# Kernel tuning notes

Hardware: AMD Instinct MI355X
Metric: run time of the kernel (lower is better)

## Reference

```python
import jax, jax.numpy as jnp
import numpy as np

B, T, C, H = 4, 4096, 2048, 128  # batch, seq, emb_dim, head_size


def setup_inputs() -> dict:
    key = jax.random.key(0)
    k1, k2, k3, k4 = jax.random.split(key, 4)
    idx = jax.random.normal(k1, (B, T, C), dtype=jnp.float32)
    # nn.Linear weight layout: [out_features, in_features]; scale like torch init
    s = 1.0 / np.sqrt(C)
    Wq = jax.random.uniform(k2, (H, C), jnp.float32, -s, s)
    Wk = jax.random.uniform(k3, (H, C), jnp.float32, -s, s)
    Wv = jax.random.uniform(k4, (H, C), jnp.float32, -s, s)
    return {"idx": idx, "Wq": Wq, "Wk": Wk, "Wv": Wv}


def reference(idx, Wq, Wk, Wv):
    b, t, c = idx.shape
    q = jnp.einsum('btc,hc->bth', idx, Wq)  # [B,T,H]
    k = jnp.einsum('btc,hc->bth', idx, Wk)
    v = jnp.einsum('btc,hc->bth', idx, Wv)
    # NOTE: original computes keys @ queries^T and scales by emb_dim**-0.5
    scale = jnp.asarray(c, idx.dtype) ** -0.5
    wei = jnp.einsum('bih,bjh->bij', k, q) * scale  # [B,T,T]
    causal = jnp.tril(jnp.ones((t, t), dtype=bool))
    wei = jnp.where(causal, wei, -jnp.inf)
    wei = jax.nn.softmax(wei, axis=-1)
    return jnp.einsum('bij,bjh->bih', wei, v)  # [B,T,H]
```

## Files before the change

kernel.cpp:

```cpp
#include <hip/hip_runtime.h>
#include <hip/hip_bf16.h>
#include <cstdint>

#define TSEQ 4096
#define CDIM 2048
#define HDIM 128

typedef short bf8v __attribute__((ext_vector_type(8)));
typedef float f4v  __attribute__((ext_vector_type(4)));

__device__ __forceinline__ unsigned short f2b(float f) {
  union { float f; unsigned u; } v; v.f = f;
  unsigned u = v.u;
  return (unsigned short)((u + 0x7fffu + ((u >> 16) & 1u)) >> 16);
}

__device__ __forceinline__ f4v mfma16(bf8v a, bf8v b, f4v c) {
  return __builtin_amdgcn_mfma_f32_16x16x32_bf16(a, b, c, 0, 0, 0);
}

__global__ void wcat_kernel(const float* __restrict__ Wq, const float* __restrict__ Wk,
                            const float* __restrict__ Wv, unsigned short* __restrict__ Wcat) {
  int e = (blockIdx.x * 256 + threadIdx.x) * 4;
  int n = e >> 11;
  int k = e & 2047;
  const float* src;
  if (n < 128)      src = Wq + (size_t)n * CDIM + k;
  else if (n < 256) src = Wk + (size_t)(n - 128) * CDIM + k;
  else              src = Wv + (size_t)(n - 256) * CDIM + k;
  float4 f = *(const float4*)src;
  ushort4 o;
  o.x = f2b(f.x); o.y = f2b(f.y); o.z = f2b(f.z); o.w = f2b(f.w);
  *(ushort4*)(Wcat + e) = o;
}

__global__ __launch_bounds__(256, 4) void proj_gemm(const float* __restrict__ A,
                                                    const unsigned short* __restrict__ Bw,
                                                    unsigned short* __restrict__ QB,
                                                    unsigned short* __restrict__ KA,
                                                    unsigned short* __restrict__ VB) {
  __shared__ union {
    struct { unsigned short As[2][64][40]; unsigned short Bs[2][128][40]; } st;
    unsigned short Ct[64][132];
  } sm;
  const int m0 = blockIdx.x * 64;
  const int y  = blockIdx.y;
  const int n0 = y * 128;
  const int tid = threadIdx.x;
  const int lane = tid & 63;
  const int w = tid >> 6;
  const int wm = (w & 1) * 32, wn = (w >> 1) * 64;
  const int llo = lane & 15, lhi = lane >> 4;

  f4v acc[2][4];
#pragma unroll
  for (int i = 0; i < 2; ++i)
#pragma unroll
    for (int j = 0; j < 4; ++j) acc[i][j] = (f4v){0.f, 0.f, 0.f, 0.f};

  const int arow = tid >> 2, acol = (tid & 3) * 8;
  const int brow = tid >> 1, bcol = (tid & 1) * 16;
  const float* aptr = A + (size_t)(m0 + arow) * CDIM + acol;
  const unsigned short* bptr = Bw + (size_t)(n0 + brow) * CDIM + bcol;

  float4 fa0 = *(const float4*)(aptr);
  float4 fa1 = *(const float4*)(aptr + 4);
  uint4  ub0 = *(const uint4*)(bptr);
  uint4  ub1 = *(const uint4*)(bptr + 8);
  {
    ushort4 o0, o1;
    o0.x = f2b(fa0.x); o0.y = f2b(fa0.y); o0.z = f2b(fa0.z); o0.w = f2b(fa0.w);
    o1.x = f2b(fa1.x); o1.y = f2b(fa1.y); o1.z = f2b(fa1.z); o1.w = f2b(fa1.w);
    *(ushort4*)&sm.st.As[0][arow][acol]     = o0;
    *(ushort4*)&sm.st.As[0][arow][acol + 4] = o1;
    *(uint4*)&sm.st.Bs[0][brow][bcol]     = ub0;
    *(uint4*)&sm.st.Bs[0][brow][bcol + 8] = ub1;
  }

  for (int it = 0; it < 64; ++it) {
    const int cur = it & 1;
    __syncthreads();
    if (it < 63) {
      const float* ap = aptr + (it + 1) * 32;
      fa0 = *(const float4*)(ap);
      fa1 = *(const float4*)(ap + 4);
      const unsigned short* bp = bptr + (it + 1) * 32;
      ub0 = *(const uint4*)(bp);
      ub1 = *(const uint4*)(bp + 8);
    }
    bf8v af[2], bfr[4];
    af[0] = *(const bf8v*)&sm.st.As[cur][wm + llo][lhi * 8];
    af[1] = *(const bf8v*)&sm.st.As[cur][wm + 16 + llo][lhi * 8];
#pragma unroll
    for (int j = 0; j < 4; ++j)
      bfr[j] = *(const bf8v*)&sm.st.Bs[cur][wn + j * 16 + llo][lhi * 8];
#pragma unroll
    for (int i = 0; i < 2; ++i)
#pragma unroll
      for (int j = 0; j < 4; ++j) acc[i][j] = mfma16(af[i], bfr[j], acc[i][j]);
    if (it < 63) {
      ushort4 o0, o1;
      o0.x = f2b(fa0.x); o0.y = f2b(fa0.y); o0.z = f2b(fa0.z); o0.w = f2b(fa0.w);
      o1.x = f2b(fa1.x); o1.y = f2b(fa1.y); o1.z = f2b(fa1.z); o1.w = f2b(fa1.w);
      int nxt = cur ^ 1;
      *(ushort4*)&sm.st.As[nxt][arow][acol]     = o0;
      *(ushort4*)&sm.st.As[nxt][arow][acol + 4] = o1;
      *(uint4*)&sm.st.Bs[nxt][brow][bcol]     = ub0;
      *(uint4*)&sm.st.Bs[nxt][brow][bcol + 8] = ub1;
    }
  }
  __syncthreads();
#pragma unroll
  for (int i = 0; i < 2; ++i)
#pragma unroll
    for (int j = 0; j < 4; ++j)
#pragma unroll
      for (int r = 0; r < 4; ++r)
        sm.Ct[wm + i * 16 + lhi * 4 + r][wn + j * 16 + llo] = f2b(acc[i][j][r]);
  __syncthreads();
  if (y < 2) {
    unsigned short* dst = (y == 0) ? QB : KA;
    const size_t base16 = (size_t)(m0 >> 4);
#pragma unroll
    for (int p = 0; p < 4; ++p) {
      int g = p * 256 + tid;
      int t16l = g >> 8, kk = (g >> 6) & 3, ln = g & 63;
      int lo = ln & 15, hi = ln >> 4;
      bf8v v = *(const bf8v*)&sm.Ct[t16l * 16 + lo][kk * 32 + hi * 8];
      *(bf8v*)(dst + (((base16 + t16l) * 4 + kk) * 64 + ln) * 8) = v;
    }
  } else {
    const size_t base32 = (size_t)(m0 >> 5);
#pragma unroll
    for (int p = 0; p < 5; ++p) {
      int g = p * 256 + tid;
      if (g < 1152) {
        int jbl = g / 576;
        int ht  = (g % 576) >> 6;
        int ln  = g & 63;
        int lo = ln & 15, hi = ln >> 4;
        bf8v v;
        if (ht == 8) {
#pragma unroll
          for (int e = 0; e < 8; ++e) v[e] = (lo == 0) ? (short)0x3F80 : (short)0;
        } else {
#pragma unroll
          for (int e = 0; e < 8; ++e) v[e] = (short)sm.Ct[jbl * 32 + hi * 8 + e][ht * 16 + lo];
        }
        *(bf8v*)(VB + (((base32 + jbl) * 9 + ht) * 512 + (size_t)ln * 8)) = v;
      }
    }
  }
}

__global__ __launch_bounds__(256, 4) void attn4(const unsigned short* __restrict__ QB,
                                                const unsigned short* __restrict__ KA,
                                                const unsigned short* __restrict__ VB,
                                                float* __restrict__ out) {
  __shared__ union SM {
    unsigned short Ps[4][16][68];
    struct { float Om[4][16][68]; float Lm[4][16]; } mg;
  } sm;
  const int x = blockIdx.x;
  const int b = x & 3;
  const int u = x >> 2;
  const int g = u >> 6, r0 = u & 63;
  const int s = (g & 1) ? (g * 64 + 63 - r0) : (g * 64 + r0);
  const int lastjt = s >> 2;
  const int tid = threadIdx.x;
  const int w = tid >> 6, lane = tid & 63;
  const int llo = lane & 15, lhi = lane >> 4;
  const float scale = 0.022097086912079608f;

  bf8v aK[4];
  {
    const unsigned short* kp = KA + (size_t)(b * 256 + s) * 2048;
#pragma unroll
    for (int kk = 0; kk < 4; ++kk) aK[kk] = *(const bf8v*)(kp + (kk * 64 + lane) * 8);
  }

  f4v Oacc[9];
#pragma unroll
  for (int nt = 0; nt < 9; ++nt) Oacc[nt] = (f4v){0.f, 0.f, 0.f, 0.f};

  for (int jt = w; jt <= lastjt; jt += 4) {
    const unsigned short* qp = QB + (size_t)(b * 256 + jt * 4) * 2048;
#pragma unroll
    for (int ct = 0; ct < 4; ++ct) {
      f4v acc = (f4v){0.f, 0.f, 0.f, 0.f};
#pragma unroll
      for (int kk = 0; kk < 4; ++kk) {
        bf8v bq = *(const bf8v*)(qp + ((ct * 4 + kk) * 64 + lane) * 8);
        acc = mfma16(aK[kk], bq, acc);
      }
#pragma unroll
      for (int r = 0; r < 4; ++r) {
        float sv = acc[r];
        if (jt == lastjt) {
          int j = jt * 64 + ct * 16 + llo;
          int i = s * 16 + lhi * 4 + r;
          if (j > i) sv = -3.0e38f;
        }
        sm.Ps[w][lhi * 4 + r][ct * 16 + llo] = f2b(__expf(sv * scale));
      }
    }
    bf8v aP[2];
    aP[0] = *(const bf8v*)&sm.Ps[w][llo][lhi * 8];
    aP[1] = *(const bf8v*)&sm.Ps[w][llo][32 + lhi * 8];
    const unsigned short* vp = VB + (size_t)(b * 128 + jt * 2) * 4608;
#pragma unroll
    for (int nt = 0; nt < 9; ++nt) {
      f4v o = Oacc[nt];
#pragma unroll
      for (int kk = 0; kk < 2; ++kk) {
        bf8v bv = *(const bf8v*)(vp + kk * 4608 + nt * 512 + (size_t)lane * 8);
        o = mfma16(aP[kk], bv, o);
      }
      Oacc[nt] = o;
    }
  }

#pragma unroll
  for (int half = 0; half < 2; ++half) {
    __syncthreads();
#pragma unroll
    for (int nt = 0; nt < 4; ++nt)
#pragma unroll
      for (int r = 0; r < 4; ++r)
        sm.mg.Om[w][lhi * 4 + r][nt * 16 + llo] = Oacc[half * 4 + nt][r];
    if (half == 0 && llo == 0) {
#pragma unroll
      for (int r = 0; r < 4; ++r) sm.mg.Lm[w][lhi * 4 + r] = Oacc[8][r];
    }
    __syncthreads();
    {
      int row = tid >> 4, c0 = (tid & 15) * 4;
      float L = sm.mg.Lm[0][row] + sm.mg.Lm[1][row] + sm.mg.Lm[2][row] + sm.mg.Lm[3][row];
      float inv = 1.0f / L;
      float* op = out + (size_t)(b * TSEQ + s * 16 + row) * HDIM + half * 64 + c0;
#pragma unroll
      for (int e = 0; e < 4; ++e) {
        float o = sm.mg.Om[0][row][c0 + e] + sm.mg.Om[1][row][c0 + e] +
                  sm.mg.Om[2][row][c0 + e] + sm.mg.Om[3][row][c0 + e];
        op[e] = o * inv;
      }
    }
  }
}

extern "C" void kernel_launch(void* const* d_in, const int* in_sizes, int n_in,
                              void* d_out, int out_size, void* d_ws, size_t ws_size,
                              hipStream_t stream) {
  const float* idx = (const float*)d_in[0];
  const float* Wq  = (const float*)d_in[1];
  const float* Wk  = (const float*)d_in[2];
  const float* Wv  = (const float*)d_in[3];
  float* out = (float*)d_out;
  char* ws = (char*)d_ws;
  unsigned short* Wcat = (unsigned short*)ws;
  unsigned short* QB   = (unsigned short*)(ws + ((size_t)2  << 20));
  unsigned short* KA   = (unsigned short*)(ws + ((size_t)7  << 20));
  unsigned short* VB   = (unsigned short*)(ws + ((size_t)12 << 20));

  wcat_kernel<<<768, 256, 0, stream>>>(Wq, Wk, Wv, Wcat);
  proj_gemm<<<dim3(256, 3), 256, 0, stream>>>(idx, Wcat, QB, KA, VB);
  attn4<<<1024, 256, 0, stream>>>(QB, KA, VB, out);
}
```

Before: 331.5 us.

## Double waves per block in projection GEMM and attention kernels

Both the projection GEMM and the attention kernel move from 256 to 512 threads per block. In the GEMM each of 8 waves now computes a 32x32 sub-tile instead of 32x64, and each thread loads half as much per k-step. In attention the key tiles are strided across 8 waves instead of 4, and the final merge sums 8 partial outputs and denominators through shared memory. The aim is more in-flight waves to hide memory and MFMA latency and shorter per-block serial loops. The cost is less register-level reuse per wave in the GEMM, more shared memory, and a larger cross-wave reduction.

New measurement: 347.1 us. 1.05x slower.

```diff
diff --git a/kernel.cpp b/kernel.cpp
--- a/kernel.cpp
+++ b/kernel.cpp
@@ -34,7 +34,7 @@
   *(ushort4*)(Wcat + e) = o;
 }
 
-__global__ __launch_bounds__(256, 4) void proj_gemm(const float* __restrict__ A,
+__global__ __launch_bounds__(512, 6) void proj_gemm(const float* __restrict__ A,
                                                     const unsigned short* __restrict__ Bw,
                                                     unsigned short* __restrict__ QB,
                                                     unsigned short* __restrict__ KA,
@@ -49,71 +49,58 @@
   const int tid = threadIdx.x;
   const int lane = tid & 63;
   const int w = tid >> 6;
-  const int wm = (w & 1) * 32, wn = (w >> 1) * 64;
+  const int wm = (w & 1) * 32, wn = (w >> 1) * 32;
   const int llo = lane & 15, lhi = lane >> 4;
 
-  f4v acc[2][4];
+  f4v acc[2][2];
 #pragma unroll
   for (int i = 0; i < 2; ++i)
 #pragma unroll
-    for (int j = 0; j < 4; ++j) acc[i][j] = (f4v){0.f, 0.f, 0.f, 0.f};
-
-  const int arow = tid >> 2, acol = (tid & 3) * 8;
-  const int brow = tid >> 1, bcol = (tid & 1) * 16;
+    for (int j = 0; j < 2; ++j) acc[i][j] = (f4v){0.f, 0.f, 0.f, 0.f};
+
+  const int arow = tid >> 3, acol = (tid & 7) * 4;
+  const int brow = tid >> 2, bcol = (tid & 3) * 8;
   const float* aptr = A + (size_t)(m0 + arow) * CDIM + acol;
   const unsigned short* bptr = Bw + (size_t)(n0 + brow) * CDIM + bcol;
 
-  float4 fa0 = *(const float4*)(aptr);
-  float4 fa1 = *(const float4*)(aptr + 4);
-  uint4  ub0 = *(const uint4*)(bptr);
-  uint4  ub1 = *(const uint4*)(bptr + 8);
+  float4 fa = *(const float4*)(aptr);
+  uint4  ub = *(const uint4*)(bptr);
   {
-    ushort4 o0, o1;
-    o0.x = f2b(fa0.x); o0.y = f2b(fa0.y); o0.z = f2b(fa0.z); o0.w = f2b(fa0.w);
-    o1.x = f2b(fa1.x); o1.y = f2b(fa1.y); o1.z = f2b(fa1.z); o1.w = f2b(fa1.w);
-    *(ushort4*)&sm.st.As[0][arow][acol]     = o0;
-    *(ushort4*)&sm.st.As[0][arow][acol + 4] = o1;
-    *(uint4*)&sm.st.Bs[0][brow][bcol]     = ub0;
-    *(uint4*)&sm.st.Bs[0][brow][bcol + 8] = ub1;
+    ushort4 o;
+    o.x = f2b(fa.x); o.y = f2b(fa.y); o.z = f2b(fa.z); o.w = f2b(fa.w);
+    *(ushort4*)&sm.st.As[0][arow][acol] = o;
+    *(uint4*)&sm.st.Bs[0][brow][bcol]   = ub;
   }
 
   for (int it = 0; it < 64; ++it) {
     const int cur = it & 1;
     __syncthreads();
     if (it < 63) {
-      const float* ap = aptr + (it + 1) * 32;
-      fa0 = *(const float4*)(ap);
-      fa1 = *(const float4*)(ap + 4);
-      const unsigned short* bp = bptr + (it + 1) * 32;
-      ub0 = *(const uint4*)(bp);
-      ub1 = *(const uint4*)(bp + 8);
-    }
-    bf8v af[2], bfr[4];
-    af[0] = *(const bf8v*)&sm.st.As[cur][wm + llo][lhi * 8];
-    af[1] = *(const bf8v*)&sm.st.As[cur][wm + 16 + llo][lhi * 8];
-#pragma unroll
-    for (int j = 0; j < 4; ++j)
-      bfr[j] = *(const bf8v*)&sm.st.Bs[cur][wn + j * 16 + llo][lhi * 8];
+      fa = *(const float4*)(aptr + (it + 1) * 32);
+      ub = *(const uint4*)(bptr + (it + 1) * 32);
+    }
+    bf8v af[2], bfr[2];
+    af[0]  = *(const bf8v*)&sm.st.As[cur][wm + llo][lhi * 8];
+    af[1]  = *(const bf8v*)&sm.st.As[cur][wm + 16 + llo][lhi * 8];
+    bfr[0] = *(const bf8v*)&sm.st.Bs[cur][wn + llo][lhi * 8];
+    bfr[1] = *(const bf8v*)&sm.st.Bs[cur][wn + 16 + llo][lhi * 8];
 #pragma unroll
     for (int i = 0; i < 2; ++i)
 #pragma unroll
-      for (int j = 0; j < 4; ++j) acc[i][j] = mfma16(af[i], bfr[j], acc[i][j]);
+      for (int j = 0; j < 2; ++j) acc[i][j] = mfma16(af[i], bfr[j], acc[i][j]);
     if (it < 63) {
-      ushort4 o0, o1;
-      o0.x = f2b(fa0.x); o0.y = f2b(fa0.y); o0.z = f2b(fa0.z); o0.w = f2b(fa0.w);
-      o1.x = f2b(fa1.x); o1.y = f2b(fa1.y); o1.z = f2b(fa1.z); o1.w = f2b(fa1.w);
+      ushort4 o;
+      o.x = f2b(fa.x); o.y = f2b(fa.y); o.z = f2b(fa.z); o.w = f2b(fa.w);
       int nxt = cur ^ 1;
-      *(ushort4*)&sm.st.As[nxt][arow][acol]     = o0;
-      *(ushort4*)&sm.st.As[nxt][arow][acol + 4] = o1;
-      *(uint4*)&sm.st.Bs[nxt][brow][bcol]     = ub0;
-      *(uint4*)&sm.st.Bs[nxt][brow][bcol + 8] = ub1;
+      *(ushort4*)&sm.st.As[nxt][arow][acol] = o;
+      *(uint4*)&sm.st.Bs[nxt][brow][bcol]   = ub;
     }
   }
   __syncthreads();
 #pragma unroll
   for (int i = 0; i < 2; ++i)
 #pragma unroll
-    for (int j = 0; j < 4; ++j)
+    for (int j = 0; j < 2; ++j)
 #pragma unroll
       for (int r = 0; r < 4; ++r)
         sm.Ct[wm + i * 16 + lhi * 4 + r][wn + j * 16 + llo] = f2b(acc[i][j][r]);
@@ -122,8 +109,8 @@
     unsigned short* dst = (y == 0) ? QB : KA;
     const size_t base16 = (size_t)(m0 >> 4);
 #pragma unroll
-    for (int p = 0; p < 4; ++p) {
-      int g = p * 256 + tid;
+    for (int p = 0; p < 2; ++p) {
+      int g = p * 512 + tid;
       int t16l = g >> 8, kk = (g >> 6) & 3, ln = g & 63;
       int lo = ln & 15, hi = ln >> 4;
       bf8v v = *(const bf8v*)&sm.Ct[t16l * 16 + lo][kk * 32 + hi * 8];
@@ -132,8 +119,8 @@
   } else {
     const size_t base32 = (size_t)(m0 >> 5);
 #pragma unroll
-    for (int p = 0; p < 5; ++p) {
-      int g = p * 256 + tid;
+    for (int p = 0; p < 3; ++p) {
+      int g = p * 512 + tid;
       if (g < 1152) {
         int jbl = g / 576;
         int ht  = (g % 576) >> 6;
@@ -153,13 +140,13 @@
   }
 }
 
-__global__ __launch_bounds__(256, 4) void attn4(const unsigned short* __restrict__ QB,
+__global__ __launch_bounds__(512, 8) void attn5(const unsigned short* __restrict__ QB,
                                                 const unsigned short* __restrict__ KA,
                                                 const unsigned short* __restrict__ VB,
                                                 float* __restrict__ out) {
   __shared__ union SM {
-    unsigned short Ps[4][16][68];
-    struct { float Om[4][16][68]; float Lm[4][16]; } mg;
+    unsigned short Ps[8][16][68];
+    struct { float Om[8][16][66]; float Lm[8][16]; } mg;
   } sm;
   const int x = blockIdx.x;
   const int b = x & 3;
@@ -183,7 +170,7 @@
 #pragma unroll
   for (int nt = 0; nt < 9; ++nt) Oacc[nt] = (f4v){0.f, 0.f, 0.f, 0.f};
 
-  for (int jt = w; jt <= lastjt; jt += 4) {
+  for (int jt = w; jt <= lastjt; jt += 8) {
     const unsigned short* qp = QB + (size_t)(b * 256 + jt * 4) * 2048;
 #pragma unroll
     for (int ct = 0; ct < 4; ++ct) {
@@ -234,16 +221,20 @@
     }
     __syncthreads();
     {
-      int row = tid >> 4, c0 = (tid & 15) * 4;
-      float L = sm.mg.Lm[0][row] + sm.mg.Lm[1][row] + sm.mg.Lm[2][row] + sm.mg.Lm[3][row];
+      int row = tid >> 5, c0 = (tid & 31) * 2;
+      float L = 0.f;
+#pragma unroll
+      for (int ww = 0; ww < 8; ++ww) L += sm.mg.Lm[ww][row];
       float inv = 1.0f / L;
+      float o0 = 0.f, o1 = 0.f;
+#pragma unroll
+      for (int ww = 0; ww < 8; ++ww) {
+        o0 += sm.mg.Om[ww][row][c0];
+        o1 += sm.mg.Om[ww][row][c0 + 1];
+      }
       float* op = out + (size_t)(b * TSEQ + s * 16 + row) * HDIM + half * 64 + c0;
-#pragma unroll
-      for (int e = 0; e < 4; ++e) {
-        float o = sm.mg.Om[0][row][c0 + e] + sm.mg.Om[1][row][c0 + e] +
-                  sm.mg.Om[2][row][c0 + e] + sm.mg.Om[3][row][c0 + e];
-        op[e] = o * inv;
-      }
+      op[0] = o0 * inv;
+      op[1] = o1 * inv;
     }
   }
 }
@@ -263,6 +254,6 @@
   unsigned short* VB   = (unsigned short*)(ws + ((size_t)12 << 20));
 
   wcat_kernel<<<768, 256, 0, stream>>>(Wq, Wk, Wv, Wcat);
-  proj_gemm<<<dim3(256, 3), 256, 0, stream>>>(idx, Wcat, QB, KA, VB);
-  attn4<<<1024, 256, 0, stream>>>(QB, KA, VB, out);
-}
+  proj_gemm<<<dim3(256, 3), 512, 0, stream>>>(idx, Wcat, QB, KA, VB);
+  attn5<<<1024, 512, 0, stream>>>(QB, KA, VB, out);
+}
```
